# Performance work log

Hardware: AMD Instinct MI355X
Metric: run time of the kernel (lower is better)

Reference implementation:

```python
import jax, jax.numpy as jnp
import numpy as np

NUM_GRAPHS = 1024
IN_F = 256
HID = 512


def setup_inputs() -> dict:
    key = jax.random.key(0)
    ks = jax.random.split(key, 20)
    s_in = 1.0 / np.sqrt(IN_F)
    s_h = 1.0 / np.sqrt(HID)
    inp = {
        "x": jax.random.normal(ks[0], (200000, IN_F), dtype=jnp.float32),
        "batch": jnp.sort(jax.random.randint(ks[1], (200000,), 0, NUM_GRAPHS)),
        # transforms: Linear(in_features -> hidden)
        "W_mean": jax.random.uniform(ks[2], (IN_F, HID), jnp.float32, -s_in, s_in),
        "b_mean": jax.random.uniform(ks[3], (HID,), jnp.float32, -s_in, s_in),
        "W_max": jax.random.uniform(ks[4], (IN_F, HID), jnp.float32, -s_in, s_in),
        "b_max": jax.random.uniform(ks[5], (HID,), jnp.float32, -s_in, s_in),
        "W_sum": jax.random.uniform(ks[6], (IN_F, HID), jnp.float32, -s_in, s_in),
        "b_sum": jax.random.uniform(ks[7], (HID,), jnp.float32, -s_in, s_in),
        # gates: Linear(hidden -> 1) + sigmoid
        "g_mean_w": jax.random.uniform(ks[8], (HID, 1), jnp.float32, -s_h, s_h),
        "g_mean_b": jax.random.uniform(ks[9], (1,), jnp.float32, -s_h, s_h),
        "g_max_w": jax.random.uniform(ks[10], (HID, 1), jnp.float32, -s_h, s_h),
        "g_max_b": jax.random.uniform(ks[11], (1,), jnp.float32, -s_h, s_h),
        "g_sum_w": jax.random.uniform(ks[12], (HID, 1), jnp.float32, -s_h, s_h),
        "g_sum_b": jax.random.uniform(ks[13], (1,), jnp.float32, -s_h, s_h),
        # output proj: Linear(hidden -> in_features)
        "W_out": jax.random.uniform(ks[14], (HID, IN_F), jnp.float32, -s_h, s_h),
        "b_out": jax.random.uniform(ks[15], (IN_F,), jnp.float32, -s_h, s_h),
        # layer norm params
        "ln_gamma": jnp.ones((IN_F,), jnp.float32),
        "ln_beta": jnp.zeros((IN_F,), jnp.float32),
    }
    return inp


def reference(x, batch, W_mean, b_mean, W_max, b_max, W_sum, b_sum,
              g_mean_w, g_mean_b, g_max_w, g_max_b, g_sum_w, g_sum_b,
              W_out, b_out, ln_gamma, ln_beta):
    # --- segment pools over node dim ---
    sum_pool = jax.ops.segment_sum(x, batch, num_segments=NUM_GRAPHS)  # [G, F]
    counts = jax.ops.segment_sum(jnp.ones((x.shape[0],), x.dtype), batch,
                                 num_segments=NUM_GRAPHS)  # [G]
    mean_pool = sum_pool / jnp.maximum(counts, 1.0)[:, None]
    max_pool = jax.ops.segment_max(x, batch, num_segments=NUM_GRAPHS)
    max_pool = jnp.where(counts[:, None] > 0, max_pool, 0.0)

    # --- per-pool linear transforms ---
    mean_repr = mean_pool @ W_mean + b_mean  # [G, H]
    max_repr = max_pool @ W_max + b_max
    sum_repr = sum_pool @ W_sum + b_sum

    # --- gated fusion ---
    g_mean = jax.nn.sigmoid(mean_repr @ g_mean_w + g_mean_b)  # [G, 1]
    g_max = jax.nn.sigmoid(max_repr @ g_max_w + g_max_b)
    g_sum = jax.nn.sigmoid(sum_repr @ g_sum_w + g_sum_b)
    gates = jax.nn.softmax(jnp.concatenate([g_mean, g_max, g_sum], axis=1), axis=1)
    pooled = (gates[:, 0:1] * mean_repr + gates[:, 1:2] * max_repr
              + gates[:, 2:3] * sum_repr)

    # --- output projection (+dropout as eval identity) + layer norm ---
    emb = pooled @ W_out + b_out  # [G, F]
    mu = jnp.mean(emb, axis=-1, keepdims=True)
    var = jnp.var(emb, axis=-1, keepdims=True)
    emb = (emb - mu) * jax.lax.rsqrt(var + 1e-5) * ln_gamma + ln_beta
    return emb
```

## Files before the change

### kernel.cpp

```cpp
#include <hip/hip_runtime.h>
#include <math.h>

#define NUM_GRAPHS 1024
#define IN_F 256
#define HID 512

typedef __bf16 bf16x4 __attribute__((ext_vector_type(4)));
typedef __bf16 bf16x8 __attribute__((ext_vector_type(8)));
typedef float  f32x4  __attribute__((ext_vector_type(4)));

__device__ __forceinline__ int wave_lower_bound(const int* __restrict__ b, int n, int v, int lane) {
    int lo = 0, hi = n;
    while (lo < hi) {
        int stride = (hi - lo + 63) >> 6;
        int idx = lo + lane * stride;
        bool pred = (idx < hi) && (b[idx] < v);
        unsigned long long bal = __ballot(pred);
        int cnt = __popcll(bal);
        int nhi = lo + cnt * stride;
        lo = (cnt == 0) ? lo : lo + (cnt - 1) * stride + 1;
        hi = (nhi < hi) ? nhi : hi;
    }
    return lo;
}

__device__ __forceinline__ float bdot8(bf16x8 a, float4 w0, float4 w1) {
    return (float)a[0]*w0.x + (float)a[1]*w0.y + (float)a[2]*w0.z + (float)a[3]*w0.w
         + (float)a[4]*w1.x + (float)a[5]*w1.y + (float)a[6]*w1.z + (float)a[7]*w1.w;
}

__global__ __launch_bounds__(256) void pool_prep_kernel(
    const float* __restrict__ x, const int* __restrict__ batch, int N,
    __bf16* __restrict__ pool_mean, __bf16* __restrict__ pool_max,
    __bf16* __restrict__ pool_sum,
    const float* __restrict__ Wm, const float* __restrict__ Wx, const float* __restrict__ Wsm,
    const float* __restrict__ Wout,
    __bf16* __restrict__ wt,
    __bf16* __restrict__ wtout)
{
    if (blockIdx.x >= NUM_GRAPHS) {
        __shared__ float tile[64][65];
        int tb = blockIdx.x - NUM_GRAPHS;
        int z = tb >> 5, t = tb & 31;
        const float* S; __bf16* D; int SC, SR, r0, cb;
        if (z < 3) {
            S = (z==0) ? Wm : (z==1) ? Wx : Wsm;
            D = wt + (size_t)z * HID * IN_F;
            SR = 256; SC = 512;
            r0 = (t >> 3) * 64; cb = (t & 7) * 64;
        } else {
            S = Wout; D = wtout;
            SR = 512; SC = 256;
            r0 = (t >> 2) * 64; cb = (t & 3) * 64;
        }
        int r  = threadIdx.x >> 2;
        int c0 = (threadIdx.x & 3) * 16;
        #pragma unroll
        for (int j = 0; j < 4; ++j) {
            float4 v = *(const float4*)&S[(size_t)(r0 + r)*SC + cb + c0 + j*4];
            tile[r][c0+j*4+0] = v.x; tile[r][c0+j*4+1] = v.y;
            tile[r][c0+j*4+2] = v.z; tile[r][c0+j*4+3] = v.w;
        }
        __syncthreads();
        #pragma unroll
        for (int j = 0; j < 4; ++j) {
            bf16x4 o;
            o.x = (__bf16)tile[c0+j*4+0][r];
            o.y = (__bf16)tile[c0+j*4+1][r];
            o.z = (__bf16)tile[c0+j*4+2][r];
            o.w = (__bf16)tile[c0+j*4+3][r];
            *(bf16x4*)&D[(size_t)(cb + r)*SR + r0 + c0 + j*4] = o;
        }
        return;
    }
    int g = blockIdx.x;
    int w = threadIdx.x >> 6, lane = threadIdx.x & 63;
    __shared__ int sb[2];
    if (w < 2) {
        int lb = wave_lower_bound(batch, N, g + w, lane);
        if (lane == 0) sb[w] = lb;
    }
    __syncthreads();
    int start = sb[0], end = sb[1];
    int cnt = end - start;
    const float4* x4 = (const float4*)x;
    float4 s = make_float4(0.f, 0.f, 0.f, 0.f);
    float4 m = make_float4(-INFINITY, -INFINITY, -INFINITY, -INFINITY);
    int r = start + w;
    for (; r + 12 < end; r += 16) {
        float4 v0 = x4[(size_t)(r     )*64 + lane];
        float4 v1 = x4[(size_t)(r +  4)*64 + lane];
        float4 v2 = x4[(size_t)(r +  8)*64 + lane];
        float4 v3 = x4[(size_t)(r + 12)*64 + lane];
        s.x += (v0.x+v1.x)+(v2.x+v3.x); s.y += (v0.y+v1.y)+(v2.y+v3.y);
        s.z += (v0.z+v1.z)+(v2.z+v3.z); s.w += (v0.w+v1.w)+(v2.w+v3.w);
        m.x = fmaxf(m.x, fmaxf(fmaxf(v0.x,v1.x), fmaxf(v2.x,v3.x)));
        m.y = fmaxf(m.y, fmaxf(fmaxf(v0.y,v1.y), fmaxf(v2.y,v3.y)));
        m.z = fmaxf(m.z, fmaxf(fmaxf(v0.z,v1.z), fmaxf(v2.z,v3.z)));
        m.w = fmaxf(m.w, fmaxf(fmaxf(v0.w,v1.w), fmaxf(v2.w,v3.w)));
    }
    for (; r < end; r += 4) {
        float4 v = x4[(size_t)r*64 + lane];
        s.x += v.x; s.y += v.y; s.z += v.z; s.w += v.w;
        m.x = fmaxf(m.x, v.x); m.y = fmaxf(m.y, v.y);
        m.z = fmaxf(m.z, v.z); m.w = fmaxf(m.w, v.w);
    }
    __shared__ float4 Ls[4][64];
    __shared__ float4 Lm[4][64];
    Ls[w][lane] = s; Lm[w][lane] = m;
    __syncthreads();
    if (w == 0) {
        float4 s0 = Ls[0][lane], s1 = Ls[1][lane], s2 = Ls[2][lane], s3 = Ls[3][lane];
        float4 m0 = Lm[0][lane], m1 = Lm[1][lane], m2 = Lm[2][lane], m3 = Lm[3][lane];
        float4 st, mt;
        st.x = (s0.x+s1.x)+(s2.x+s3.x); st.y = (s0.y+s1.y)+(s2.y+s3.y);
        st.z = (s0.z+s1.z)+(s2.z+s3.z); st.w = (s0.w+s1.w)+(s2.w+s3.w);
        mt.x = fmaxf(fmaxf(m0.x,m1.x), fmaxf(m2.x,m3.x));
        mt.y = fmaxf(fmaxf(m0.y,m1.y), fmaxf(m2.y,m3.y));
        mt.z = fmaxf(fmaxf(m0.z,m1.z), fmaxf(m2.z,m3.z));
        mt.w = fmaxf(fmaxf(m0.w,m1.w), fmaxf(m2.w,m3.w));
        float inv = 1.0f / fmaxf((float)cnt, 1.0f);
        if (cnt == 0) mt = make_float4(0.f, 0.f, 0.f, 0.f);
        bf16x4 sb4, mb4, xb4;
        sb4.x = (__bf16)st.x;       sb4.y = (__bf16)st.y;
        sb4.z = (__bf16)st.z;       sb4.w = (__bf16)st.w;
        mb4.x = (__bf16)(st.x*inv); mb4.y = (__bf16)(st.y*inv);
        mb4.z = (__bf16)(st.z*inv); mb4.w = (__bf16)(st.w*inv);
        xb4.x = (__bf16)mt.x;       xb4.y = (__bf16)mt.y;
        xb4.z = (__bf16)mt.z;       xb4.w = (__bf16)mt.w;
        size_t o = (size_t)g*64 + lane;
        ((bf16x4*)pool_sum)[o]  = sb4;
        ((bf16x4*)pool_mean)[o] = mb4;
        ((bf16x4*)pool_max)[o]  = xb4;
    }
}

__global__ __launch_bounds__(256) void transform_mfma(
    const __bf16* __restrict__ pm, const __bf16* __restrict__ px, const __bf16* __restrict__ ps,
    const __bf16* __restrict__ wtm, const __bf16* __restrict__ wtx, const __bf16* __restrict__ wts,
    const float* __restrict__ bm_, const float* __restrict__ bx_, const float* __restrict__ bs_,
    __bf16* __restrict__ r_mean, __bf16* __restrict__ r_max, __bf16* __restrict__ r_sum)
{
    int z = blockIdx.z;
    const __bf16* A  = (z==0) ? pm  : (z==1) ? px  : ps;
    const __bf16* Bt = (z==0) ? wtm : (z==1) ? wtx : wts;
    const float* bias= (z==0) ? bm_ : (z==1) ? bx_ : bs_;
    __bf16* R        = (z==0) ? r_mean : (z==1) ? r_max : r_sum;

    int bn0 = blockIdx.x * 64;
    int bm0 = blockIdx.y * 64;
    int w = threadIdx.x >> 6, lane = threadIdx.x & 63;
    int qm = lane >> 4, rm = lane & 15;
    const bf16x8* Arow = (const bf16x8*)(A + (size_t)(bm0 + w*16 + rm)*IN_F);
    const bf16x8* B0 = (const bf16x8*)(Bt + (size_t)(bn0 +  0 + rm)*IN_F);
    const bf16x8* B1 = (const bf16x8*)(Bt + (size_t)(bn0 + 16 + rm)*IN_F);
    const bf16x8* B2 = (const bf16x8*)(Bt + (size_t)(bn0 + 32 + rm)*IN_F);
    const bf16x8* B3 = (const bf16x8*)(Bt + (size_t)(bn0 + 48 + rm)*IN_F);
    f32x4 a0 = {0.f,0.f,0.f,0.f}, a1 = a0, a2 = a0, a3 = a0;
    #pragma unroll
    for (int j = 0; j < 8; ++j) {
        int fi = j*4 + qm;
        bf16x8 af = Arow[fi];
        a0 = __builtin_amdgcn_mfma_f32_16x16x32_bf16(af, B0[fi], a0, 0, 0, 0);
        a1 = __builtin_amdgcn_mfma_f32_16x16x32_bf16(af, B1[fi], a1, 0, 0, 0);
        a2 = __builtin_amdgcn_mfma_f32_16x16x32_bf16(af, B2[fi], a2, 0, 0, 0);
        a3 = __builtin_amdgcn_mfma_f32_16x16x32_bf16(af, B3[fi], a3, 0, 0, 0);
    }
    int row0 = bm0 + w*16 + qm*4;
    float b0 = bias[bn0 +  0 + rm], b1 = bias[bn0 + 16 + rm];
    float b2 = bias[bn0 + 32 + rm], b3 = bias[bn0 + 48 + rm];
    #pragma unroll
    for (int r = 0; r < 4; ++r) {
        __bf16* Rr = R + (size_t)(row0 + r)*HID;
        Rr[bn0 +  0 + rm] = (__bf16)(a0[r] + b0);
        Rr[bn0 + 16 + rm] = (__bf16)(a1[r] + b1);
        Rr[bn0 + 32 + rm] = (__bf16)(a2[r] + b2);
        Rr[bn0 + 48 + rm] = (__bf16)(a3[r] + b3);
    }
}

#define EM 16
__global__ __launch_bounds__(256) void fused_tail(
    const __bf16* __restrict__ r_mean, const __bf16* __restrict__ r_max, const __bf16* __restrict__ r_sum,
    const float* __restrict__ gwm, const float* __restrict__ gbm,
    const float* __restrict__ gwx, const float* __restrict__ gbx,
    const float* __restrict__ gws, const float* __restrict__ gbs,
    const __bf16* __restrict__ wtout, const float* __restrict__ bout,
    const float* __restrict__ gamma, const float* __restrict__ beta,
    float* __restrict__ out)
{
    int g0 = blockIdx.x * EM;
    int tid = threadIdx.x;
    int w = tid >> 6, lane = tid & 63;
    int qm = lane >> 4, rm = lane & 15;

    __shared__ __align__(16) char smem_raw[3*EM*HID*2];
    __bf16 (*R3)[EM][HID] = (__bf16(*)[EM][HID])smem_raw;
    float (*Es)[264] = (float(*)[264])smem_raw;
    __shared__ __bf16 pooled[EM][520];
    __shared__ float wgt[EM][3];

    #pragma unroll
    for (int i = 0; i < 12; ++i) {
        int c = tid + i*256;
        int z = c >> 10, rem = c & 1023;
        int g = rem >> 6, kc = (rem & 63) * 8;
        const __bf16* src = (z==0) ? r_mean : (z==1) ? r_max : r_sum;
        *(bf16x8*)&R3[z][g][kc] = *(const bf16x8*)&src[(size_t)(g0 + g)*HID + kc];
    }
    __syncthreads();

    float4 wm0 = *(const float4*)&gwm[lane*8], wm1 = *(const float4*)&gwm[lane*8+4];
    float4 wx0 = *(const float4*)&gwx[lane*8], wx1 = *(const float4*)&gwx[lane*8+4];
    float4 ws0 = *(const float4*)&gws[lane*8], ws1 = *(const float4*)&gws[lane*8+4];
    #pragma unroll
    for (int gi = 0; gi < 4; ++gi) {
        int g = w*4 + gi;
        bf16x8 am = *(const bf16x8*)&R3[0][g][lane*8];
        bf16x8 ax = *(const bf16x8*)&R3[1][g][lane*8];
        bf16x8 as = *(const bf16x8*)&R3[2][g][lane*8];
        float dm  = bdot8(am, wm0, wm1);
        float dx  = bdot8(ax, wx0, wx1);
        float dsv = bdot8(as, ws0, ws1);
        #pragma unroll
        for (int off = 32; off > 0; off >>= 1) {
            dm  += __shfl_xor(dm,  off, 64);
            dx  += __shfl_xor(dx,  off, 64);
            dsv += __shfl_xor(dsv, off, 64);
        }
        if (lane == 0) {
            float sm = 1.f/(1.f + expf(-(dm  + gbm[0])));
            float sx = 1.f/(1.f + expf(-(dx  + gbx[0])));
            float ss = 1.f/(1.f + expf(-(dsv + gbs[0])));
            float em = expf(sm), ex = expf(sx), es = expf(ss);
            float inv = 1.f/(em + ex + es);
            wgt[g][0] = em*inv; wgt[g][1] = ex*inv; wgt[g][2] = es*inv;
        }
    }
    __syncthreads();

    #pragma unroll
    for (int i = 0; i < 4; ++i) {
        int c = tid + i*256;
        int g = c >> 6, kc = (c & 63) * 8;
        bf16x8 am = *(const bf16x8*)&R3[0][g][kc];
        bf16x8 ax = *(const bf16x8*)&R3[1][g][kc];
        bf16x8 as = *(const bf16x8*)&R3[2][g][kc];
        float w0 = wgt[g][0], w1 = wgt[g][1], w2 = wgt[g][2];
        bf16x8 o;
        #pragma unroll
        for (int e = 0; e < 8; ++e)
            o[e] = (__bf16)(w0*(float)am[e] + w1*(float)ax[e] + w2*(float)as[e]);
        *(bf16x8*)&pooled[g][kc] = o;
    }
    __syncthreads();

    f32x4 ac0 = {0.f,0.f,0.f,0.f}, ac1 = ac0, ac2 = ac0, ac3 = ac0;
    const __bf16* Bt0 = wtout + (size_t)((w*4+0)*16 + rm)*HID;
    const __bf16* Bt1 = wtout + (size_t)((w*4+1)*16 + rm)*HID;
    const __bf16* Bt2 = wtout + (size_t)((w*4+2)*16 + rm)*HID;
    const __bf16* Bt3 = wtout + (size_t)((w*4+3)*16 + rm)*HID;
    #pragma unroll
    for (int kk = 0; kk < 16; ++kk) {
        int ko = kk*32 + qm*8;
        bf16x8 af = *(const bf16x8*)&pooled[rm][ko];
        ac0 = __builtin_amdgcn_mfma_f32_16x16x32_bf16(af, *(const bf16x8*)&Bt0[ko], ac0, 0, 0, 0);
        ac1 = __builtin_amdgcn_mfma_f32_16x16x32_bf16(af, *(const bf16x8*)&Bt1[ko], ac1, 0, 0, 0);
        ac2 = __builtin_amdgcn_mfma_f32_16x16x32_bf16(af, *(const bf16x8*)&Bt2[ko], ac2, 0, 0, 0);
        ac3 = __builtin_amdgcn_mfma_f32_16x16x32_bf16(af, *(const bf16x8*)&Bt3[ko], ac3, 0, 0, 0);
    }
    __syncthreads();

    float bo0 = bout[(w*4+0)*16 + rm], bo1 = bout[(w*4+1)*16 + rm];
    float bo2 = bout[(w*4+2)*16 + rm], bo3 = bout[(w*4+3)*16 + rm];
    #pragma unroll
    for (int r = 0; r < 4; ++r) {
        int g = qm*4 + r;
        Es[g][(w*4+0)*16 + rm] = ac0[r] + bo0;
        Es[g][(w*4+1)*16 + rm] = ac1[r] + bo1;
        Es[g][(w*4+2)*16 + rm] = ac2[r] + bo2;
        Es[g][(w*4+3)*16 + rm] = ac3[r] + bo3;
    }
    __syncthreads();

    float4 ga = *(const float4*)&gamma[lane*4];
    float4 be = *(const float4*)&beta[lane*4];
    #pragma unroll
    for (int i = 0; i < 4; ++i) {
        int g = w*4 + i;
        float4 v = *(const float4*)&Es[g][lane*4];
        float s  = (v.x + v.y) + (v.z + v.w);
        float sq = (v.x*v.x + v.y*v.y) + (v.z*v.z + v.w*v.w);
        #pragma unroll
        for (int off = 32; off > 0; off >>= 1) {
            s  += __shfl_xor(s,  off, 64);
            sq += __shfl_xor(sq, off, 64);
        }
        float mu  = s * (1.0f/IN_F);
        float var = sq * (1.0f/IN_F) - mu*mu;
        float rs  = rsqrtf(var + 1e-5f);
        float4 o;
        o.x = (v.x - mu)*rs*ga.x + be.x;
        o.y = (v.y - mu)*rs*ga.y + be.y;
        o.z = (v.z - mu)*rs*ga.z + be.z;
        o.w = (v.w - mu)*rs*ga.w + be.w;
        *(float4*)&out[(size_t)(g0 + g)*IN_F + lane*4] = o;
    }
}

extern "C" void kernel_launch(void* const* d_in, const int* in_sizes, int n_in,
                              void* d_out, int out_size, void* d_ws, size_t ws_size,
                              hipStream_t stream)
{
    const float* x        = (const float*)d_in[0];
    const int*   batch    = (const int*)d_in[1];
    const float* W_mean   = (const float*)d_in[2];
    const float* b_mean   = (const float*)d_in[3];
    const float* W_max    = (const float*)d_in[4];
    const float* b_max    = (const float*)d_in[5];
    const float* W_sum    = (const float*)d_in[6];
    const float* b_sum    = (const float*)d_in[7];
    const float* g_mean_w = (const float*)d_in[8];
    const float* g_mean_b = (const float*)d_in[9];
    const float* g_max_w  = (const float*)d_in[10];
    const float* g_max_b  = (const float*)d_in[11];
    const float* g_sum_w  = (const float*)d_in[12];
    const float* g_sum_b  = (const float*)d_in[13];
    const float* W_out    = (const float*)d_in[14];
    const float* b_out    = (const float*)d_in[15];
    const float* ln_gamma = (const float*)d_in[16];
    const float* ln_beta  = (const float*)d_in[17];
    float* out = (float*)d_out;
    int N = in_sizes[1];

    __bf16* B = (__bf16*)d_ws;
    __bf16* pm    = B;
    __bf16* px    = pm  + (size_t)NUM_GRAPHS*IN_F;
    __bf16* psu   = px  + (size_t)NUM_GRAPHS*IN_F;
    __bf16* wtm   = psu + (size_t)NUM_GRAPHS*IN_F;
    __bf16* wtx   = wtm + (size_t)HID*IN_F;
    __bf16* wts   = wtx + (size_t)HID*IN_F;
    __bf16* wtout = wts + (size_t)HID*IN_F;
    __bf16* r_mean = wtout + (size_t)IN_F*HID;
    __bf16* r_max  = r_mean + (size_t)NUM_GRAPHS*HID;
    __bf16* r_sum  = r_max  + (size_t)NUM_GRAPHS*HID;

    pool_prep_kernel<<<NUM_GRAPHS + 128, 256, 0, stream>>>(
        x, batch, N, pm, px, psu,
        W_mean, W_max, W_sum, W_out, wtm, wtout);

    dim3 gridC(HID/64, NUM_GRAPHS/64, 3);
    transform_mfma<<<gridC, 256, 0, stream>>>(pm, px, psu, wtm, wtx, wts,
                                              b_mean, b_max, b_sum,
                                              r_mean, r_max, r_sum);

    fused_tail<<<NUM_GRAPHS/EM, 256, 0, stream>>>(r_mean, r_max, r_sum,
                                                  g_mean_w, g_mean_b, g_max_w, g_max_b,
                                                  g_sum_w, g_sum_b,
                                                  wtout, b_out, ln_gamma, ln_beta, out);
}
```

Baseline: 342.1 us.

## Shrink GEMM and tail tiles to double block counts for occupancy

The transform GEMM tile drops from 64x64 to 32x64 with a 2x2 wave layout, doubling its grid. The fused tail now handles 8 graphs per block instead of 16, also doubling its grid, and zero-pads the unused MFMA rows of the pooled buffer. The goal is more parallelism for these small kernels, which run well below a full GPU with 1024 graphs. The cost is more redundant weight reads per block and wasted half-MFMA work in the tail.

```diff
diff --git a/kernel.cpp b/kernel.cpp
--- a/kernel.cpp
+++ b/kernel.cpp
@@ -148,38 +148,33 @@
     __bf16* R        = (z==0) ? r_mean : (z==1) ? r_max : r_sum;
 
     int bn0 = blockIdx.x * 64;
-    int bm0 = blockIdx.y * 64;
+    int bm0 = blockIdx.y * 32;
     int w = threadIdx.x >> 6, lane = threadIdx.x & 63;
+    int wm = w & 1, wn = w >> 1;
     int qm = lane >> 4, rm = lane & 15;
-    const bf16x8* Arow = (const bf16x8*)(A + (size_t)(bm0 + w*16 + rm)*IN_F);
-    const bf16x8* B0 = (const bf16x8*)(Bt + (size_t)(bn0 +  0 + rm)*IN_F);
-    const bf16x8* B1 = (const bf16x8*)(Bt + (size_t)(bn0 + 16 + rm)*IN_F);
-    const bf16x8* B2 = (const bf16x8*)(Bt + (size_t)(bn0 + 32 + rm)*IN_F);
-    const bf16x8* B3 = (const bf16x8*)(Bt + (size_t)(bn0 + 48 + rm)*IN_F);
-    f32x4 a0 = {0.f,0.f,0.f,0.f}, a1 = a0, a2 = a0, a3 = a0;
+    const bf16x8* Arow = (const bf16x8*)(A + (size_t)(bm0 + wm*16 + rm)*IN_F);
+    const bf16x8* B0 = (const bf16x8*)(Bt + (size_t)(bn0 + wn*32 +  0 + rm)*IN_F);
+    const bf16x8* B1 = (const bf16x8*)(Bt + (size_t)(bn0 + wn*32 + 16 + rm)*IN_F);
+    f32x4 a0 = {0.f,0.f,0.f,0.f}, a1 = a0;
     #pragma unroll
     for (int j = 0; j < 8; ++j) {
         int fi = j*4 + qm;
         bf16x8 af = Arow[fi];
         a0 = __builtin_amdgcn_mfma_f32_16x16x32_bf16(af, B0[fi], a0, 0, 0, 0);
         a1 = __builtin_amdgcn_mfma_f32_16x16x32_bf16(af, B1[fi], a1, 0, 0, 0);
-        a2 = __builtin_amdgcn_mfma_f32_16x16x32_bf16(af, B2[fi], a2, 0, 0, 0);
-        a3 = __builtin_amdgcn_mfma_f32_16x16x32_bf16(af, B3[fi], a3, 0, 0, 0);
-    }
-    int row0 = bm0 + w*16 + qm*4;
-    float b0 = bias[bn0 +  0 + rm], b1 = bias[bn0 + 16 + rm];
-    float b2 = bias[bn0 + 32 + rm], b3 = bias[bn0 + 48 + rm];
+    }
+    int row0 = bm0 + wm*16 + qm*4;
+    float b0 = bias[bn0 + wn*32 +  0 + rm];
+    float b1 = bias[bn0 + wn*32 + 16 + rm];
     #pragma unroll
     for (int r = 0; r < 4; ++r) {
         __bf16* Rr = R + (size_t)(row0 + r)*HID;
-        Rr[bn0 +  0 + rm] = (__bf16)(a0[r] + b0);
-        Rr[bn0 + 16 + rm] = (__bf16)(a1[r] + b1);
-        Rr[bn0 + 32 + rm] = (__bf16)(a2[r] + b2);
-        Rr[bn0 + 48 + rm] = (__bf16)(a3[r] + b3);
-    }
-}
-
-#define EM 16
+        Rr[bn0 + wn*32 +  0 + rm] = (__bf16)(a0[r] + b0);
+        Rr[bn0 + wn*32 + 16 + rm] = (__bf16)(a1[r] + b1);
+    }
+}
+
+#define EM 8
 __global__ __launch_bounds__(256) void fused_tail(
     const __bf16* __restrict__ r_mean, const __bf16* __restrict__ r_max, const __bf16* __restrict__ r_sum,
     const float* __restrict__ gwm, const float* __restrict__ gbm,
@@ -197,25 +192,33 @@
     __shared__ __align__(16) char smem_raw[3*EM*HID*2];
     __bf16 (*R3)[EM][HID] = (__bf16(*)[EM][HID])smem_raw;
     float (*Es)[264] = (float(*)[264])smem_raw;
-    __shared__ __bf16 pooled[EM][520];
+    __shared__ __bf16 pooled[16][520];
     __shared__ float wgt[EM][3];
 
     #pragma unroll
-    for (int i = 0; i < 12; ++i) {
+    for (int i = 0; i < 6; ++i) {
         int c = tid + i*256;
-        int z = c >> 10, rem = c & 1023;
+        int z = c >> 9, rem = c & 511;
         int g = rem >> 6, kc = (rem & 63) * 8;
         const __bf16* src = (z==0) ? r_mean : (z==1) ? r_max : r_sum;
         *(bf16x8*)&R3[z][g][kc] = *(const bf16x8*)&src[(size_t)(g0 + g)*HID + kc];
     }
+    #pragma unroll
+    for (int i = 0; i < 3; ++i) {
+        int c = tid + i*256;
+        if (c < 520) {
+            bf16x8 zr = {};
+            *(bf16x8*)&pooled[8 + c/65][(c%65)*8] = zr;
+        }
+    }
     __syncthreads();
 
     float4 wm0 = *(const float4*)&gwm[lane*8], wm1 = *(const float4*)&gwm[lane*8+4];
     float4 wx0 = *(const float4*)&gwx[lane*8], wx1 = *(const float4*)&gwx[lane*8+4];
     float4 ws0 = *(const float4*)&gws[lane*8], ws1 = *(const float4*)&gws[lane*8+4];
     #pragma unroll
-    for (int gi = 0; gi < 4; ++gi) {
-        int g = w*4 + gi;
+    for (int gi = 0; gi < 2; ++gi) {
+        int g = w*2 + gi;
         bf16x8 am = *(const bf16x8*)&R3[0][g][lane*8];
         bf16x8 ax = *(const bf16x8*)&R3[1][g][lane*8];
         bf16x8 as = *(const bf16x8*)&R3[2][g][lane*8];
@@ -240,7 +243,7 @@
     __syncthreads();
 
     #pragma unroll
-    for (int i = 0; i < 4; ++i) {
+    for (int i = 0; i < 2; ++i) {
         int c = tid + i*256;
         int g = c >> 6, kc = (c & 63) * 8;
         bf16x8 am = *(const bf16x8*)&R3[0][g][kc];
@@ -273,21 +276,23 @@
 
     float bo0 = bout[(w*4+0)*16 + rm], bo1 = bout[(w*4+1)*16 + rm];
     float bo2 = bout[(w*4+2)*16 + rm], bo3 = bout[(w*4+3)*16 + rm];
-    #pragma unroll
-    for (int r = 0; r < 4; ++r) {
-        int g = qm*4 + r;
-        Es[g][(w*4+0)*16 + rm] = ac0[r] + bo0;
-        Es[g][(w*4+1)*16 + rm] = ac1[r] + bo1;
-        Es[g][(w*4+2)*16 + rm] = ac2[r] + bo2;
-        Es[g][(w*4+3)*16 + rm] = ac3[r] + bo3;
+    if (qm < 2) {
+        #pragma unroll
+        for (int r = 0; r < 4; ++r) {
+            int g = qm*4 + r;
+            Es[g][(w*4+0)*16 + rm] = ac0[r] + bo0;
+            Es[g][(w*4+1)*16 + rm] = ac1[r] + bo1;
+            Es[g][(w*4+2)*16 + rm] = ac2[r] + bo2;
+            Es[g][(w*4+3)*16 + rm] = ac3[r] + bo3;
+        }
     }
     __syncthreads();
 
     float4 ga = *(const float4*)&gamma[lane*4];
     float4 be = *(const float4*)&beta[lane*4];
     #pragma unroll
-    for (int i = 0; i < 4; ++i) {
-        int g = w*4 + i;
+    for (int i = 0; i < 2; ++i) {
+        int g = w*2 + i;
         float4 v = *(const float4*)&Es[g][lane*4];
         float s  = (v.x + v.y) + (v.z + v.w);
         float sq = (v.x*v.x + v.y*v.y) + (v.z*v.z + v.w*v.w);
@@ -349,7 +354,7 @@
         x, batch, N, pm, px, psu,
         W_mean, W_max, W_sum, W_out, wtm, wtout);
 
-    dim3 gridC(HID/64, NUM_GRAPHS/64, 3);
+    dim3 gridC(HID/64, NUM_GRAPHS/32, 3);
     transform_mfma<<<gridC, 256, 0, stream>>>(pm, px, psu, wtm, wtx, wts,
                                               b_mean, b_max, b_sum,
                                               r_mean, r_max, r_sum);
```

Result: no change. 336.4 us (-1.7%).
